# Kernel tuning notes

Hardware: AMD Instinct MI355X
Metric: run time of the kernel (lower is better)

Reference implementation:

```python
import jax, jax.numpy as jnp
import numpy as np

BATCH, SEQ, D = 128, 256, 64


def setup_inputs() -> dict:
    key = jax.random.key(0)
    k1, k2, k3 = jax.random.split(key, 3)
    eye = jnp.eye(D, dtype=jnp.float32)
    return {
        "x": jax.random.normal(k1, (BATCH, D), dtype=jnp.float32),
        "U_t": jax.random.normal(k2, (BATCH, SEQ, D), dtype=jnp.float32),
        "Y_t": jax.random.normal(k3, (BATCH, SEQ, D), dtype=jnp.float32),
        # learnable params, 'identity' init per module
        "F_mat": eye,
        "B_mat": eye,
        "H": eye,
        "LQ": jnp.tril(eye),
        "LR": jnp.tril(eye),
    }


def _kalman(x, U_t, Y_t, F_mat, B_mat, H, LQ, LR):
    d = x.shape[-1]
    bsz = x.shape[0]
    Q = LQ @ LQ.T                      # [D,D] process noise cov
    R = LR @ LR.T                      # [D,D] measurement noise cov
    I = jnp.eye(d, dtype=x.dtype)
    P0 = jnp.broadcast_to(I, (bsz, d, d))

    def step(carry, inp):
        x_prev, P = carry              # [B,D], [B,D,D]
        u, y = inp                     # [B,D], [B,D,D]
        x_pred = x_prev @ F_mat.T + u @ B_mat.T
        P_pred = F_mat @ P @ F_mat.T + Q            # broadcasts [D,D]@[B,D,D]
        S = H @ P_pred @ H.T + R                    # [B,D,D]
        S_inv = jnp.linalg.inv(S)
        K = P_pred @ (H.T @ S_inv)                  # Kalman gain [B,D,D]
        innov = y - x_pred @ H.T                    # [B,D]
        # matches torch: (innov.unsqueeze(1) @ K).squeeze(1)
        x_new = x_pred + jnp.einsum('bd,bde->be', innov, K)
        IKH = I - K @ H
        P_new = IKH @ P_pred @ jnp.swapaxes(IKH, -1, -2) \
              + K @ R @ jnp.swapaxes(K, -1, -2)
        P_new = 0.5 * (P_new + jnp.swapaxes(P_new, -1, -2))  # symmetrize
        return (x_new, P_new), (x_new, P_new)

    inputs = (jnp.swapaxes(U_t, 0, 1), jnp.swapaxes(Y_t, 0, 1))  # [S,B,D]
    _, (preds, covs) = jax.lax.scan(step, (x, P0), inputs)
    # prediction [B,S,D], covariance [B,S,D,D]
    return jnp.swapaxes(preds, 0, 1), jnp.swapaxes(covs, 0, 1)


def reference(x, U_t, Y_t, F_mat, B_mat, H, LQ, LR):
    return _kalman(x, U_t, Y_t, F_mat, B_mat, H, LQ, LR)
```

## Files before the change

### kernel.cpp

```cpp
#include <hip/hip_runtime.h>

#define BATCH 128
#define SEQ   256

#define WS_K  16
#define WS_A  (16 + SEQ * 4096)
#define WS_BP (WS_A + 4096)
#define WS_KS (WS_BP + 4096)

typedef unsigned short u16;
typedef float  f32x4v __attribute__((ext_vector_type(4)));
typedef __bf16 bf16x8 __attribute__((ext_vector_type(8)));
typedef unsigned short u16x8 __attribute__((ext_vector_type(8)));

struct Acc { f32x4v t[2][2]; };

__device__ __forceinline__ u16 bf16hi(float x) {
  unsigned u = __float_as_uint(x);
  return (u16)((u + 0x7fffu + ((u >> 16) & 1u)) >> 16);
}
__device__ __forceinline__ float bf16f(u16 h) {
  return __uint_as_float(((unsigned)h) << 16);
}

__device__ __forceinline__ int swadr(int a, int c) {
  return a * 64 + ((c ^ (a & 7)) << 3);
}

__device__ __forceinline__ bf16x8 frag(const u16* M, int strip, int kb, int q, int ln) {
  return *(const bf16x8*)(M + swadr(strip * 16 + ln, kb * 4 + q));
}

__device__ __forceinline__ void mm(const u16* As, const u16* Bs, Acc& acc,
                                   int R, int Cb, int q, int ln) {
#pragma unroll
  for (int kb = 0; kb < 2; ++kb) {
    bf16x8 ah[2], al[2], bh[2], bl[2];
#pragma unroll
    for (int i = 0; i < 2; ++i) {
      ah[i] = frag(As,        2 * R  + i, kb, q, ln);
      al[i] = frag(As + 4096, 2 * R  + i, kb, q, ln);
      bh[i] = frag(Bs,        2 * Cb + i, kb, q, ln);
      bl[i] = frag(Bs + 4096, 2 * Cb + i, kb, q, ln);
    }
#pragma unroll
    for (int i = 0; i < 2; ++i)
#pragma unroll
      for (int j = 0; j < 2; ++j) {
        acc.t[i][j] = __builtin_amdgcn_mfma_f32_16x16x32_bf16(ah[i], bh[j], acc.t[i][j], 0, 0, 0);
        acc.t[i][j] = __builtin_amdgcn_mfma_f32_16x16x32_bf16(ah[i], bl[j], acc.t[i][j], 0, 0, 0);
        acc.t[i][j] = __builtin_amdgcn_mfma_f32_16x16x32_bf16(al[i], bh[j], acc.t[i][j], 0, 0, 0);
      }
  }
}

__device__ __forceinline__ Acc accZero() {
  Acc a;
#pragma unroll
  for (int i = 0; i < 2; ++i)
#pragma unroll
    for (int j = 0; j < 2; ++j) {
      f32x4v z; z.x = 0.f; z.y = 0.f; z.z = 0.f; z.w = 0.f;
      a.t[i][j] = z;
    }
  return a;
}

__device__ __forceinline__ void storeC(float* dst, const Acc& a, int R, int Cb, int q, int ln) {
#pragma unroll
  for (int i = 0; i < 2; ++i)
#pragma unroll
    for (int j = 0; j < 2; ++j)
#pragma unroll
      for (int k = 0; k < 4; ++k)
        dst[(32 * R + 16 * i + 4 * q + k) * 64 + 32 * Cb + 16 * j + ln] = a.t[i][j][k];
}

__device__ __forceinline__ void emit16(const float* v, int row, int cb, u16* Rs, u16* Ts) {
  u16 h[16], lo[16];
#pragma unroll
  for (int e = 0; e < 16; ++e) {
    h[e] = bf16hi(v[e]);
    lo[e] = bf16hi(v[e] - bf16f(h[e]));
  }
  if (Rs) {
#pragma unroll
    for (int c = 0; c < 2; ++c) {
      u16x8 vh, vl;
#pragma unroll
      for (int e = 0; e < 8; ++e) { vh[e] = h[8 * c + e]; vl[e] = lo[8 * c + e]; }
      const int ad = swadr(row, (cb >> 3) + c);
      *(u16x8*)(Rs + ad) = vh;
      *(u16x8*)(Rs + 4096 + ad) = vl;
    }
  }
  if (Ts) {
    const int rc = row >> 3, rr = row & 7;
#pragma unroll
    for (int e = 0; e < 16; ++e) {
      const int a = cb + e;
      const int ad = a * 64 + ((rc ^ (a & 7)) << 3) + rr;
      Ts[ad] = h[e];
      Ts[4096 + ad] = lo[e];
    }
  }
}

__device__ __forceinline__ void splitsrc(const float* src, u16* Rs, u16* Ts,
                                         int mode, float scale, float dval, int tid) {
  const int row = tid >> 2, cb = (tid & 3) << 4;
  float v[16];
#pragma unroll
  for (int m = 0; m < 4; ++m) {
    f32x4v x = *(const f32x4v*)(src + row * 64 + cb + 4 * m);
    v[4 * m] = x.x; v[4 * m + 1] = x.y; v[4 * m + 2] = x.z; v[4 * m + 3] = x.w;
  }
  if (mode == 1) {
#pragma unroll
    for (int e = 0; e < 16; ++e) v[e] *= scale;
  } else if (mode == 2) {
#pragma unroll
    for (int e = 0; e < 16; ++e) v[e] = (((cb + e) == row) ? dval : 0.f) - v[e];
  }
  emit16(v, row, cb, Rs, Ts);
}

__device__ __forceinline__ float redmax(float v, float* red, int tid) {
#pragma unroll
  for (int off = 32; off > 0; off >>= 1) v = fmaxf(v, __shfl_xor(v, off));
  if ((tid & 63) == 0) red[300 + (tid >> 6)] = v;
  __syncthreads();
  float m = fmaxf(fmaxf(red[300], red[301]), fmaxf(red[302], red[303]));
  __syncthreads();
  return m;
}

__device__ __forceinline__ float dot4(float4 a, float4 b, float acc) {
  return fmaf(a.x, b.x, fmaf(a.y, b.y, fmaf(a.z, b.z, fmaf(a.w, b.w, acc))));
}

__global__ void __launch_bounds__(256, 1)
k1_riccati(const float* __restrict__ Fg, const float* __restrict__ Bg,
           const float* __restrict__ Hg, const float* __restrict__ LQg,
           const float* __restrict__ LRg, float* __restrict__ ws,
           float* __restrict__ covs) {
  __shared__ __align__(16) u16 smb[7 * 8192];
  __shared__ __align__(16) float Mf32[4096];
  __shared__ __align__(16) float Ppf32[4096];
  __shared__ __align__(16) float red[308];

  const int tid = threadIdx.x;
  const int l = tid & 63, w = tid >> 6, q = l >> 4, ln = l & 15;
  const int R = w >> 1, Cb = w & 1;

  {
    const int row = tid >> 2, cb = (tid & 3) << 4;
    float od = 0.f;
    const float* mats[5] = {Fg, Bg, Hg, LQg, LRg};
#pragma unroll
    for (int mi = 0; mi < 5; ++mi) {
      const float* M = mats[mi];
#pragma unroll
      for (int m = 0; m < 4; ++m) {
        f32x4v x = *(const f32x4v*)(M + row * 64 + cb + 4 * m);
        const int j0c = cb + 4 * m;
        if (j0c + 0 != row) od = fmaxf(od, fabsf(x.x));
        if (j0c + 1 != row) od = fmaxf(od, fabsf(x.y));
        if (j0c + 2 != row) od = fmaxf(od, fabsf(x.z));
        if (j0c + 3 != row) od = fmaxf(od, fabsf(x.w));
      }
    }
    const float odall = redmax(od, red, tid);
    if (odall == 0.f) {
      if (tid < 64) {
        const int e = tid;
        const float f = Fg[e * 65], b = Bg[e * 65], h = Hg[e * 65];
        const float lq = LQg[e * 65], lr = LRg[e * 65];
        const float qv = lq * lq, rv = lr * lr;
        float p = 1.f, kprev = 0.f, kcur = 0.f, om = 1.f;
        int tstar = SEQ - 1;
        for (int t = 0; t < SEQ; ++t) {
          const float pp = f * p * f + qv;
          const float s = h * pp * h + rv;
          const float k = pp * h / s;
          const float kh = k * h;
          const float omv = 1.f - kh;
          const float pn = omv * omv * pp + k * k * rv;
          float* Kt = ws + WS_K + (size_t)t * 4096 + e * 64;
          float* Ct = covs + (size_t)t * 4096 + e * 64;
          f32x4v z; z.x = 0.f; z.y = 0.f; z.z = 0.f; z.w = 0.f;
#pragma unroll
          for (int m = 0; m < 16; ++m) {
            *(f32x4v*)(Kt + 4 * m) = z;
            *(f32x4v*)(Ct + 4 * m) = z;
          }
          Kt[e] = k;
          Ct[e] = pn;
          float dk = (t == 0) ? 1e9f : fabsf(k - kprev);
#pragma unroll
          for (int off = 32; off > 0; off >>= 1) dk = fmaxf(dk, __shfl_xor(dk, off));
          p = pn; kprev = k; kcur = k; om = omv;
          if (dk < 1e-3f) { tstar = t; break; }
        }
        {
          const float astar = om * f, bpv = om * b;
          float* Ar = ws + WS_A + e * 64;
          float* Bp = ws + WS_BP + e * 64;
          float* Ks = ws + WS_KS + e * 64;
          f32x4v z; z.x = 0.f; z.y = 0.f; z.z = 0.f; z.w = 0.f;
#pragma unroll
          for (int m = 0; m < 16; ++m) {
            *(f32x4v*)(Ar + 4 * m) = z;
            *(f32x4v*)(Bp + 4 * m) = z;
            *(f32x4v*)(Ks + 4 * m) = z;
          }
          Ar[e] = astar; Bp[e] = bpv; Ks[e] = kcur;
          const float a2 = astar * astar, a4 = a2 * a2, a8 = a4 * a4;
          float a16 = fabsf(a8 * a8);
#pragma unroll
          for (int off = 32; off > 0; off >>= 1) a16 = fmaxf(a16, __shfl_xor(a16, off));
          if (e == 0) {
            ((int*)ws)[0] = tstar;
            ((int*)ws)[1] = (tstar <= 16 && a16 < 1e-5f) ? 1 : 0;
          }
        }
      }
      return;
    }
  }

  u16* SF = smb;
  u16* SH = smb + 8192;
  u16* SX = smb + 2 * 8192;
  u16* S1 = smb + 3 * 8192;
  u16* S2 = smb + 4 * 8192;
  u16* S3 = smb + 5 * 8192;
  u16* S4 = smb + 6 * 8192;

  splitsrc(Fg, SF, nullptr, 0, 0, 0, tid);
  splitsrc(Hg, SH, nullptr, 0, 0, 0, tid);
  splitsrc(LQg, S1, nullptr, 0, 0, 0, tid);
  __syncthreads();
  Acc qacc = accZero(); mm(S1, S1, qacc, R, Cb, q, ln);
  __syncthreads();
  splitsrc(LRg, S1, nullptr, 0, 0, 0, tid);
  __syncthreads();
  Acc racc = accZero(); mm(S1, S1, racc, R, Cb, q, ln);
  __syncthreads();
  {
    const int row = tid >> 2, cb = (tid & 3) << 4;
    float v[16];
#pragma unroll
    for (int e = 0; e < 16; ++e) v[e] = ((cb + e) == row) ? 1.f : 0.f;
    emit16(v, row, cb, S4, nullptr);
  }
  __syncthreads();

  int tstar = SEQ - 1;
  for (int t = 0; t < SEQ; ++t) {
    const u16* Wsrc = SF;
    if (t > 0) {
      Acc a = accZero(); mm(SF, S4, a, R, Cb, q, ln);
      storeC(Mf32, a, R, Cb, q, ln);
      __syncthreads();
      splitsrc(Mf32, S1, nullptr, 0, 0, 0, tid);
      __syncthreads();
      Wsrc = S1;
    }
    {
      Acc a = qacc; mm(Wsrc, SF, a, R, Cb, q, ln);
      storeC(Ppf32, a, R, Cb, q, ln);
      __syncthreads();
      splitsrc(Ppf32, S2, nullptr, 0, 0, 0, tid);
      __syncthreads();
    }
    {
      Acc a = accZero(); mm(SH, S2, a, R, Cb, q, ln);
      storeC(Mf32, a, R, Cb, q, ln);
      __syncthreads();
      splitsrc(Mf32, S3, S4, 0, 0, 0, tid);
      __syncthreads();
    }
    {
      Acc a = racc; mm(S3, SH, a, R, Cb, q, ln);
      storeC(Mf32, a, R, Cb, q, ln);
      __syncthreads();
      if (t == 0) {
        const int col = tid & 63, grp = tid >> 6;
        float s = 0.f;
        for (int r2 = grp * 16; r2 < grp * 16 + 16; ++r2) s += fabsf(Mf32[r2 * 64 + col]);
        red[tid] = s;
        __syncthreads();
        if (tid < 64) {
          float cs = red[tid] + red[64 + tid] + red[128 + tid] + red[192 + tid];
#pragma unroll
          for (int off = 32; off > 0; off >>= 1) cs = fmaxf(cs, __shfl_xor(cs, off));
          if (tid == 0) red[256] = 1.f / (cs * cs);
        }
        __syncthreads();
        const float sc = red[256];
        splitsrc(Mf32, SX, nullptr, 1, sc, 0, tid);
        __syncthreads();
      }
      splitsrc(Mf32, S2, nullptr, 0, 0, 0, tid);
      __syncthreads();
    }
    const int cap = (t == 0) ? 40 : 4;
    for (int it = 0; it < cap; ++it) {
      Acc e_ = accZero(); mm(S2, SX, e_, R, Cb, q, ln);
      float r = 0.f;
#pragma unroll
      for (int i = 0; i < 2; ++i)
#pragma unroll
        for (int j = 0; j < 2; ++j)
#pragma unroll
          for (int k = 0; k < 4; ++k) {
            const int gr = 32 * R + 16 * i + 4 * q + k;
            const int gc = 32 * Cb + 16 * j + ln;
            r = fmaxf(r, fabsf(e_.t[i][j][k] - ((gr == gc) ? 1.f : 0.f)));
          }
      const float rall = redmax(r, red, tid);
      if (rall < 5e-4f) break;
      storeC(Mf32, e_, R, Cb, q, ln);
      __syncthreads();
      splitsrc(Mf32, nullptr, S1, 2, 0, 2.0f, tid);
      __syncthreads();
      Acc x2 = accZero(); mm(SX, S1, x2, R, Cb, q, ln);
      storeC(Mf32, x2, R, Cb, q, ln);
      __syncthreads();
      splitsrc(Mf32, SX, nullptr, 0, 0, 0, tid);
      __syncthreads();
      if (rall * rall < 1e-4f) break;
    }
    __syncthreads();
    float dk;
    {
      Acc a = accZero(); mm(SX, S4, a, R, Cb, q, ln);
      storeC(Mf32, a, R, Cb, q, ln);
      __syncthreads();
      const int row = tid >> 2, cb = (tid & 3) << 4;
      float v[16]; float dmax = (t == 0) ? 1e9f : 0.f;
      float* wrow = ws + WS_K + (size_t)t * 4096 + row * 64 + cb;
#pragma unroll
      for (int m = 0; m < 4; ++m) {
        f32x4v x = *(const f32x4v*)(Mf32 + row * 64 + cb + 4 * m);
        v[4 * m] = x.x; v[4 * m + 1] = x.y; v[4 * m + 2] = x.z; v[4 * m + 3] = x.w;
        *(f32x4v*)(wrow + 4 * m) = x;
      }
      if (t > 0) {
        const float* prow = wrow - 4096;
#pragma unroll
        for (int m = 0; m < 4; ++m) {
          f32x4v p = *(const f32x4v*)(prow + 4 * m);
          dmax = fmaxf(dmax, fmaxf(fmaxf(fabsf(v[4 * m] - p.x), fabsf(v[4 * m + 1] - p.y)),
                                   fmaxf(fabsf(v[4 * m + 2] - p.z), fabsf(v[4 * m + 3] - p.w))));
        }
      }
      emit16(v, row, cb, nullptr, S1);
      dk = redmax(dmax, red, tid);
    }
    {
      Acc a = accZero(); mm(S1, S4, a, R, Cb, q, ln);
      storeC(Mf32, a, R, Cb, q, ln);
      __syncthreads();
      const int row = tid >> 2, cb = (tid & 3) << 4;
      float pv[16];
#pragma unroll
      for (int m = 0; m < 4; ++m) {
        f32x4v mij = *(const f32x4v*)(Mf32 + row * 64 + cb + 4 * m);
        f32x4v pp  = *(const f32x4v*)(Ppf32 + row * 64 + cb + 4 * m);
        pv[4 * m]     = pp.x - 0.5f * (mij.x + Mf32[(cb + 4 * m + 0) * 64 + row]);
        pv[4 * m + 1] = pp.y - 0.5f * (mij.y + Mf32[(cb + 4 * m + 1) * 64 + row]);
        pv[4 * m + 2] = pp.z - 0.5f * (mij.z + Mf32[(cb + 4 * m + 2) * 64 + row]);
        pv[4 * m + 3] = pp.w - 0.5f * (mij.w + Mf32[(cb + 4 * m + 3) * 64 + row]);
      }
      float* crow = covs + (size_t)t * 4096 + row * 64 + cb;
#pragma unroll
      for (int m = 0; m < 4; ++m) {
        f32x4v o; o.x = pv[4 * m]; o.y = pv[4 * m + 1]; o.z = pv[4 * m + 2]; o.w = pv[4 * m + 3];
        *(f32x4v*)(crow + 4 * m) = o;
      }
      emit16(pv, row, cb, S4, nullptr);
      __syncthreads();
    }
    if (dk < 1e-3f) { tstar = t; break; }
  }

  {
    Acc a = accZero(); mm(S1, SH, a, R, Cb, q, ln);
    storeC(Mf32, a, R, Cb, q, ln);
    __syncthreads();
    splitsrc(Mf32, S2, nullptr, 2, 0, 1.0f, tid);
    __syncthreads();
  }
  splitsrc(Fg, nullptr, S3, 0, 0, 0, tid);
  __syncthreads();
  {
    Acc a = accZero(); mm(S2, S3, a, R, Cb, q, ln);
    storeC(Mf32, a, R, Cb, q, ln);
#pragma unroll
    for (int i = 0; i < 2; ++i)
#pragma unroll
      for (int j = 0; j < 2; ++j)
#pragma unroll
        for (int k = 0; k < 4; ++k)
          ws[WS_A + (size_t)((32 * R + 16 * i + 4 * q + k) * 64 + 32 * Cb + 16 * j + ln)] = a.t[i][j][k];
    __syncthreads();
    splitsrc(Mf32, S1, S4, 0, 0, 0, tid);
    __syncthreads();
  }
  splitsrc(Bg, nullptr, S3, 0, 0, 0, tid);
  __syncthreads();
  {
    Acc a = accZero(); mm(S2, S3, a, R, Cb, q, ln);
#pragma unroll
    for (int i = 0; i < 2; ++i)
#pragma unroll
      for (int j = 0; j < 2; ++j)
#pragma unroll
        for (int k = 0; k < 4; ++k)
          ws[WS_BP + (size_t)((32 * R + 16 * i + 4 * q + k) * 64 + 32 * Cb + 16 * j + ln)] = a.t[i][j][k];
  }
  {
    const int row = tid >> 2, cb = (tid & 3) << 4;
    const float* srcr = ws + WS_K + (size_t)tstar * 4096 + row * 64 + cb;
    float* dstr = ws + WS_KS + row * 64 + cb;
#pragma unroll
    for (int m = 0; m < 4; ++m) *(f32x4v*)(dstr + 4 * m) = *(const f32x4v*)(srcr + 4 * m);
  }
  __syncthreads();
  {
    Acc a = accZero(); mm(S1, S4, a, R, Cb, q, ln);
    storeC(Mf32, a, R, Cb, q, ln); __syncthreads();
    splitsrc(Mf32, S2, S3, 0, 0, 0, tid); __syncthreads();
  }
  {
    Acc a = accZero(); mm(S2, S3, a, R, Cb, q, ln);
    storeC(Mf32, a, R, Cb, q, ln); __syncthreads();
    splitsrc(Mf32, S1, S4, 0, 0, 0, tid); __syncthreads();
  }
  {
    Acc a = accZero(); mm(S1, S4, a, R, Cb, q, ln);
    storeC(Mf32, a, R, Cb, q, ln); __syncthreads();
    splitsrc(Mf32, S2, S3, 0, 0, 0, tid); __syncthreads();
  }
  {
    Acc a = accZero(); mm(S2, S3, a, R, Cb, q, ln);
    float am = 0.f;
#pragma unroll
    for (int i = 0; i < 2; ++i)
#pragma unroll
      for (int j = 0; j < 2; ++j)
#pragma unroll
        for (int k = 0; k < 4; ++k) am = fmaxf(am, fabsf(a.t[i][j][k]));
    const float amax = redmax(am, red, tid);
    if (tid == 0) {
      ((int*)ws)[0] = tstar;
      ((int*)ws)[1] = (tstar <= 16 && amax < 1e-5f) ? 1 : 0;
    }
  }
}

#define NXWG 1024
#define NBWG 2048

__global__ void __launch_bounds__(64, 1)
k2_fused(const float* __restrict__ x0, const float* __restrict__ U,
         const float* __restrict__ Y, const float* __restrict__ Fg,
         const float* __restrict__ Bg, const float* __restrict__ Hg,
         const float* __restrict__ ws, float* __restrict__ preds,
         float* __restrict__ covs) {
  const int e = threadIdx.x;
  const int wg = blockIdx.x;
  const int tstar = ((const int*)ws)[0];
  const int flag  = ((const int*)ws)[1];

  if (wg < NBWG) {
    const int s = wg >> 3, bg = wg & 7;
    const int se = (s < tstar) ? s : tstar;
    const float4* src = (const float4*)(covs + (size_t)se * 4096);
    float4 r[16];
#pragma unroll
    for (int j = 0; j < 16; ++j) r[j] = src[j * 64 + e];
    for (int b = bg; b < BATCH; b += 8) {
      if (b == 0 && s <= tstar) continue;
      float4* dst = (float4*)(covs + ((size_t)b * SEQ + s) * 4096);
#pragma unroll
      for (int j = 0; j < 16; ++j) dst[j * 64 + e] = r[j];
    }
  } else {
    const int xw = wg - NBWG;
    const int b = xw >> 3, c = xw & 7;
    __shared__ __align__(16) float xv[64], xp[64], inn[64], us[2][64], ys[2][64];

    if (c == 0) {
      const int t1 = flag ? 32 : SEQ;
      float4 Fr[16], Br[16], Hr[16], Kr[16];
      const float4* fp = (const float4*)(Fg + e * 64);
      const float4* bp = (const float4*)(Bg + e * 64);
      const float4* hp = (const float4*)(Hg + e * 64);
#pragma unroll
      for (int m = 0; m < 16; ++m) { Fr[m] = fp[m]; Br[m] = bp[m]; Hr[m] = hp[m]; }
      xv[e] = x0[b * 64 + e];
      int staged = -1;
      for (int t = 0; t < t1; ++t) {
        const int se = (t < tstar) ? t : tstar;
        if (se != staged) {
          const float4* kp = (const float4*)(ws + WS_K + (size_t)se * 4096 + e * 64);
#pragma unroll
          for (int m = 0; m < 16; ++m) Kr[m] = kp[m];
          staged = se;
        }
        us[0][e] = U[((size_t)b * SEQ + t) * 64 + e];
        ys[0][e] = Y[((size_t)b * SEQ + t) * 64 + e];
        __syncthreads();
        const float4* xv4 = (const float4*)xv;
        const float4* us4 = (const float4*)us[0];
        float v = 0.f;
#pragma unroll
        for (int m = 0; m < 16; ++m) {
          v = dot4(Fr[m], xv4[m], v);
          v = dot4(Br[m], us4[m], v);
        }
        xp[e] = v;
        __syncthreads();
        const float4* xp4 = (const float4*)xp;
        float w = 0.f;
#pragma unroll
        for (int m = 0; m < 16; ++m) w = dot4(Hr[m], xp4[m], w);
        inn[e] = ys[0][e] - w;
        __syncthreads();
        const float4* in4 = (const float4*)inn;
        float z = 0.f;
#pragma unroll
        for (int m = 0; m < 16; ++m) z = dot4(Kr[m], in4[m], z);
        v = v + z;
        xv[e] = v;
        preds[((size_t)b * SEQ + t) * 64 + e] = v;
        __syncthreads();
      }
    } else {
      if (!flag) return;
      const int tb = 32 * c - 16, out0 = 32 * c, t1 = 32 * c + 32;
      float4 Ar[16], Pr[16], Sr[16];
      const float4* ap = (const float4*)(ws + WS_A + e * 64);
      const float4* pp = (const float4*)(ws + WS_BP + e * 64);
      const float4* sp = (const float4*)(ws + WS_KS + e * 64);
#pragma unroll
      for (int m = 0; m < 16; ++m) { Ar[m] = ap[m]; Pr[m] = pp[m]; Sr[m] = sp[m]; }
      xv[e] = 0.f;
      float gu = U[((size_t)b * SEQ + tb) * 64 + e];
      float gy = Y[((size_t)b * SEQ + tb) * 64 + e];
      int pb = 0;
      for (int t = tb; t < t1; ++t) {
        us[pb][e] = gu; ys[pb][e] = gy;
        __syncthreads();
        if (t + 1 < t1) {
          gu = U[((size_t)b * SEQ + (t + 1)) * 64 + e];
          gy = Y[((size_t)b * SEQ + (t + 1)) * 64 + e];
        }
        const float4* xv4 = (const float4*)xv;
        const float4* us4 = (const float4*)us[pb];
        const float4* ys4 = (const float4*)ys[pb];
        float v = 0.f;
#pragma unroll
        for (int m = 0; m < 16; ++m) {
          v = dot4(Ar[m], xv4[m], v);
          v = dot4(Pr[m], us4[m], v);
          v = dot4(Sr[m], ys4[m], v);
        }
        xv[e] = v;
        if (t >= out0) preds[((size_t)b * SEQ + t) * 64 + e] = v;
        pb ^= 1;
      }
    }
  }
}

extern "C" void kernel_launch(void* const* d_in, const int* in_sizes, int n_in,
                              void* d_out, int out_size, void* d_ws, size_t ws_size,
                              hipStream_t stream) {
  (void)in_sizes; (void)n_in; (void)out_size; (void)ws_size;
  const float* x0 = (const float*)d_in[0];
  const float* U  = (const float*)d_in[1];
  const float* Y  = (const float*)d_in[2];
  const float* F  = (const float*)d_in[3];
  const float* B  = (const float*)d_in[4];
  const float* H  = (const float*)d_in[5];
  const float* LQ = (const float*)d_in[6];
  const float* LR = (const float*)d_in[7];
  float* preds = (float*)d_out;
  float* covs  = preds + (size_t)BATCH * SEQ * 64;
  float* ws    = (float*)d_ws;

  hipLaunchKernelGGL(k1_riccati, dim3(1), dim3(256), 0, stream,
                     F, B, H, LQ, LR, ws, covs);
  hipLaunchKernelGGL(k2_fused, dim3(NBWG + NXWG), dim3(64), 0, stream,
                     x0, U, Y, F, B, H, ws, preds, covs);
}
```

Before: 665.4 us.

## Split each state row across four lanes and widen workgroups to 256 threads

The sequential state-update workgroups now use 256 threads, with four lanes per output row. Each lane holds a quarter of the matrix row in registers and the partial dot products are combined with cross-lane shuffles. This shortens the serial dependency chain per time step and lowers register pressure. The covariance broadcast workgroups are also regrouped into 512 blocks of 256 threads, each writing 64 batches. The cost is extra shuffles and an added barrier in the chunked path.

```diff
diff --git a/kernel.cpp b/kernel.cpp
--- a/kernel.cpp
+++ b/kernel.cpp
@@ -461,116 +461,126 @@
   }
 }
 
-#define NXWG 1024
-#define NBWG 2048
-
-__global__ void __launch_bounds__(64, 1)
+#define NB2 512
+#define NX2 1024
+
+__global__ void __launch_bounds__(256, 4)
 k2_fused(const float* __restrict__ x0, const float* __restrict__ U,
          const float* __restrict__ Y, const float* __restrict__ Fg,
          const float* __restrict__ Bg, const float* __restrict__ Hg,
          const float* __restrict__ ws, float* __restrict__ preds,
          float* __restrict__ covs) {
-  const int e = threadIdx.x;
+  const int tid = threadIdx.x;
   const int wg = blockIdx.x;
   const int tstar = ((const int*)ws)[0];
   const int flag  = ((const int*)ws)[1];
 
-  if (wg < NBWG) {
-    const int s = wg >> 3, bg = wg & 7;
+  if (wg < NB2) {
+    const int s = wg >> 1, half = wg & 1;
     const int se = (s < tstar) ? s : tstar;
     const float4* src = (const float4*)(covs + (size_t)se * 4096);
-    float4 r[16];
-#pragma unroll
-    for (int j = 0; j < 16; ++j) r[j] = src[j * 64 + e];
-    for (int b = bg; b < BATCH; b += 8) {
+    float4 r0 = src[tid], r1 = src[256 + tid], r2 = src[512 + tid], r3 = src[768 + tid];
+    const int b0 = half << 6;
+    for (int b = b0; b < b0 + 64; ++b) {
       if (b == 0 && s <= tstar) continue;
       float4* dst = (float4*)(covs + ((size_t)b * SEQ + s) * 4096);
-#pragma unroll
-      for (int j = 0; j < 16; ++j) dst[j * 64 + e] = r[j];
+      dst[tid] = r0; dst[256 + tid] = r1; dst[512 + tid] = r2; dst[768 + tid] = r3;
     }
   } else {
-    const int xw = wg - NBWG;
-    const int b = xw >> 3, c = xw & 7;
+    const int xw = wg - NB2;
+    const int c = xw >> 7, b = xw & 127;
+    const int e = tid >> 2, q = tid & 3;
+    const int co = q << 4;
     __shared__ __align__(16) float xv[64], xp[64], inn[64], us[2][64], ys[2][64];
 
     if (c == 0) {
       const int t1 = flag ? 32 : SEQ;
-      float4 Fr[16], Br[16], Hr[16], Kr[16];
-      const float4* fp = (const float4*)(Fg + e * 64);
-      const float4* bp = (const float4*)(Bg + e * 64);
-      const float4* hp = (const float4*)(Hg + e * 64);
-#pragma unroll
-      for (int m = 0; m < 16; ++m) { Fr[m] = fp[m]; Br[m] = bp[m]; Hr[m] = hp[m]; }
-      xv[e] = x0[b * 64 + e];
+      float4 Fr[4], Br[4], Hr[4], Kr[4];
+      {
+        const float4* fp = (const float4*)(Fg + e * 64 + co);
+        const float4* bp = (const float4*)(Bg + e * 64 + co);
+        const float4* hp = (const float4*)(Hg + e * 64 + co);
+#pragma unroll
+        for (int m = 0; m < 4; ++m) { Fr[m] = fp[m]; Br[m] = bp[m]; Hr[m] = hp[m]; }
+      }
+      if (tid < 64) xv[tid] = x0[b * 64 + tid];
       int staged = -1;
       for (int t = 0; t < t1; ++t) {
         const int se = (t < tstar) ? t : tstar;
         if (se != staged) {
-          const float4* kp = (const float4*)(ws + WS_K + (size_t)se * 4096 + e * 64);
-#pragma unroll
-          for (int m = 0; m < 16; ++m) Kr[m] = kp[m];
+          const float4* kp = (const float4*)(ws + WS_K + (size_t)se * 4096 + e * 64 + co);
+#pragma unroll
+          for (int m = 0; m < 4; ++m) Kr[m] = kp[m];
           staged = se;
         }
-        us[0][e] = U[((size_t)b * SEQ + t) * 64 + e];
-        ys[0][e] = Y[((size_t)b * SEQ + t) * 64 + e];
+        if (tid < 64) us[0][tid] = U[((size_t)b * SEQ + t) * 64 + tid];
+        else if (tid < 128) ys[0][tid - 64] = Y[((size_t)b * SEQ + t) * 64 + (tid - 64)];
         __syncthreads();
         const float4* xv4 = (const float4*)xv;
         const float4* us4 = (const float4*)us[0];
         float v = 0.f;
 #pragma unroll
-        for (int m = 0; m < 16; ++m) {
-          v = dot4(Fr[m], xv4[m], v);
-          v = dot4(Br[m], us4[m], v);
-        }
-        xp[e] = v;
+        for (int m = 0; m < 4; ++m) {
+          v = dot4(Fr[m], xv4[q * 4 + m], v);
+          v = dot4(Br[m], us4[q * 4 + m], v);
+        }
+        v += __shfl_xor(v, 1); v += __shfl_xor(v, 2);
+        if (q == 0) xp[e] = v;
         __syncthreads();
         const float4* xp4 = (const float4*)xp;
-        float w = 0.f;
-#pragma unroll
-        for (int m = 0; m < 16; ++m) w = dot4(Hr[m], xp4[m], w);
-        inn[e] = ys[0][e] - w;
+        float wv = 0.f;
+#pragma unroll
+        for (int m = 0; m < 4; ++m) wv = dot4(Hr[m], xp4[q * 4 + m], wv);
+        wv += __shfl_xor(wv, 1); wv += __shfl_xor(wv, 2);
+        if (q == 0) inn[e] = ys[0][e] - wv;
         __syncthreads();
         const float4* in4 = (const float4*)inn;
         float z = 0.f;
 #pragma unroll
-        for (int m = 0; m < 16; ++m) z = dot4(Kr[m], in4[m], z);
-        v = v + z;
-        xv[e] = v;
-        preds[((size_t)b * SEQ + t) * 64 + e] = v;
-        __syncthreads();
+        for (int m = 0; m < 4; ++m) z = dot4(Kr[m], in4[q * 4 + m], z);
+        z += __shfl_xor(z, 1); z += __shfl_xor(z, 2);
+        if (q == 0) xv[e] = xp[e] + z;
+        __syncthreads();
+        if (tid < 64) preds[((size_t)b * SEQ + t) * 64 + tid] = xv[tid];
       }
     } else {
       if (!flag) return;
       const int tb = 32 * c - 16, out0 = 32 * c, t1 = 32 * c + 32;
-      float4 Ar[16], Pr[16], Sr[16];
-      const float4* ap = (const float4*)(ws + WS_A + e * 64);
-      const float4* pp = (const float4*)(ws + WS_BP + e * 64);
-      const float4* sp = (const float4*)(ws + WS_KS + e * 64);
-#pragma unroll
-      for (int m = 0; m < 16; ++m) { Ar[m] = ap[m]; Pr[m] = pp[m]; Sr[m] = sp[m]; }
-      xv[e] = 0.f;
-      float gu = U[((size_t)b * SEQ + tb) * 64 + e];
-      float gy = Y[((size_t)b * SEQ + tb) * 64 + e];
+      float4 Ar[4], Pr[4], Sr[4];
+      {
+        const float4* ap = (const float4*)(ws + WS_A + e * 64 + co);
+        const float4* pp = (const float4*)(ws + WS_BP + e * 64 + co);
+        const float4* sp = (const float4*)(ws + WS_KS + e * 64 + co);
+#pragma unroll
+        for (int m = 0; m < 4; ++m) { Ar[m] = ap[m]; Pr[m] = pp[m]; Sr[m] = sp[m]; }
+      }
+      if (tid < 64) xv[tid] = 0.f;
+      float g = 0.f;
+      if (tid < 64) g = U[((size_t)b * SEQ + tb) * 64 + tid];
+      else if (tid < 128) g = Y[((size_t)b * SEQ + tb) * 64 + (tid - 64)];
       int pb = 0;
       for (int t = tb; t < t1; ++t) {
-        us[pb][e] = gu; ys[pb][e] = gy;
+        if (tid < 64) us[pb][tid] = g;
+        else if (tid < 128) ys[pb][tid - 64] = g;
         __syncthreads();
         if (t + 1 < t1) {
-          gu = U[((size_t)b * SEQ + (t + 1)) * 64 + e];
-          gy = Y[((size_t)b * SEQ + (t + 1)) * 64 + e];
+          if (tid < 64) g = U[((size_t)b * SEQ + (t + 1)) * 64 + tid];
+          else if (tid < 128) g = Y[((size_t)b * SEQ + (t + 1)) * 64 + (tid - 64)];
         }
         const float4* xv4 = (const float4*)xv;
         const float4* us4 = (const float4*)us[pb];
         const float4* ys4 = (const float4*)ys[pb];
         float v = 0.f;
 #pragma unroll
-        for (int m = 0; m < 16; ++m) {
-          v = dot4(Ar[m], xv4[m], v);
-          v = dot4(Pr[m], us4[m], v);
-          v = dot4(Sr[m], ys4[m], v);
-        }
-        xv[e] = v;
-        if (t >= out0) preds[((size_t)b * SEQ + t) * 64 + e] = v;
+        for (int m = 0; m < 4; ++m) {
+          v = dot4(Ar[m], xv4[q * 4 + m], v);
+          v = dot4(Pr[m], us4[q * 4 + m], v);
+          v = dot4(Sr[m], ys4[q * 4 + m], v);
+        }
+        v += __shfl_xor(v, 1); v += __shfl_xor(v, 2);
+        if (t >= out0 && q == 0) preds[((size_t)b * SEQ + t) * 64 + e] = v;
+        __syncthreads();
+        if (q == 0) xv[e] = v;
         pb ^= 1;
       }
     }
@@ -595,6 +605,6 @@
 
   hipLaunchKernelGGL(k1_riccati, dim3(1), dim3(256), 0, stream,
                      F, B, H, LQ, LR, ws, covs);
-  hipLaunchKernelGGL(k2_fused, dim3(NBWG + NXWG), dim3(64), 0, stream,
+  hipLaunchKernelGGL(k2_fused, dim3(NB2 + NX2), dim3(256), 0, stream,
                      x0, U, Y, F, B, H, ws, preds, covs);
 }
```

After: 599.7 us. -9.9%, faster.
